# Kernel optimization log

Hardware: AMD Instinct MI355X
Metric: run time of the kernel (lower is better)

The kernel has to match this reference:

```python
import jax, jax.numpy as jnp
import numpy as np

NEG_FILL = -1000000.0


def setup_inputs() -> dict:
    key = jax.random.key(0)
    k1, k2, k3, k4, k5 = jax.random.split(key, 5)
    bs, sl, hd, dd = 128, 512, 1024, 512
    x = jax.random.normal(k1, (bs, sl, hd), dtype=jnp.float32)
    mask = jax.random.randint(k2, (bs, sl), 0, 2) > 0  # bool, True = masked out
    Wq = jax.random.normal(k3, (dd, hd), dtype=jnp.float32)
    bq = jax.random.normal(k4, (dd,), dtype=jnp.float32)
    vq = jax.random.normal(k5, (dd,), dtype=jnp.float32)
    return {"x": x, "mask": mask, "Wq": Wq, "bq": bq, "vq": vq}


def reference(x, mask, Wq, bq, vq):
    # key = tanh(Uq(x)): [bs, sl, dd]
    k = jnp.tanh(jnp.einsum("bsh,dh->bsd", x, Wq) + bq)
    # score = vq . key: [bs, sl]
    score = jnp.einsum("bsd,d->bs", k, vq)
    score = jnp.where(mask, NEG_FILL, score)
    weight = jax.nn.softmax(score, axis=-1)  # [bs, sl]
    # weighted sum over sequence: [bs, hd]
    res = jnp.einsum("bs,bsh->bh", weight, x)
    return res
```

## Files before the change

kernel.cpp:

```cpp
#include <hip/hip_runtime.h>
#include <stdint.h>

#define BS 128
#define SL 512
#define HD 1024
#define DD 512
#define M_TOT (BS*SL)

typedef __attribute__((ext_vector_type(8))) short short8;
typedef __attribute__((ext_vector_type(4))) float f32x4;

__device__ __forceinline__ unsigned short f32_bf16(float f) {
    union { float f; unsigned u; } v; v.f = f;
    unsigned u = v.u + 0x7FFFu + ((v.u >> 16) & 1u);
    return (unsigned short)(u >> 16);
}
__device__ __forceinline__ float bf16_f32(unsigned short h) {
    union { unsigned u; float f; } v; v.u = ((unsigned)h) << 16; return v.f;
}
__device__ __forceinline__ float fast_tanh(float x) {
    float e = __expf(2.0f * x);
    return 1.0f - 2.0f / (e + 1.0f);
}
__device__ __forceinline__ void async_lds16(const void* g, void* l) {
    __builtin_amdgcn_global_load_lds(
        (const __attribute__((address_space(1))) unsigned int*)g,
        (__attribute__((address_space(3))) unsigned int*)l, 16, 0, 0);
}

__global__ void pack_wq_kernel(const float* __restrict__ Wq,
                               unsigned short* __restrict__ P,
                               const unsigned* __restrict__ mw,
                               int* __restrict__ flag) {
    if (blockIdx.x == 0) {
        unsigned bad = 0;
        for (int i = threadIdx.x; i < 1024; i += 256) bad |= (mw[i] > 1u) ? 1u : 0u;
        if (bad) atomicExch(flag, 1);
    }
    int t = blockIdx.x * 256 + threadIdx.x;
    int d  = t >> 7;
    int h0 = (t & 127) << 3;
    const float* src = Wq + (size_t)d * HD + h0;
    union { unsigned short s[8]; uint4 v; } a, b;
#pragma unroll
    for (int j = 0; j < 8; ++j) {
        float f = src[j];
        a.s[j] = f32_bf16(f);
        b.s[j] = f32_bf16(f - bf16_f32(a.s[j]));
    }
    int nb = d >> 7, cg = (d >> 4) & 7, lr = d & 15;
    int ks = h0 >> 5, q = (h0 >> 3) & 3;
    int l = q * 16 + lr;
    size_t base = (size_t)(nb * 32 + ks) * 8192 + (size_t)(cg * 64 + l) * 8;
    *(uint4*)(P + base)        = a.v;
    *(uint4*)(P + base + 4096) = b.v;
}

__launch_bounds__(256, 3)
__global__ void score_kernel(const float* __restrict__ x,
                             const unsigned short* __restrict__ packW,
                             const float* __restrict__ bq,
                             const float* __restrict__ vq,
                             float* __restrict__ score) {
    __shared__ unsigned short A_hi[4096];
    __shared__ unsigned short A_lo[4096];
    __shared__ unsigned short Bt[8192];

    const int bid = blockIdx.x;
    const int xcd = bid & 7;
    const int slot = bid >> 3;
    const int nb = slot & 3;
    const int m0 = (xcd + ((slot >> 2) << 3)) << 7;

    const int t = threadIdx.x;
    const int l = t & 63;
    const int w = t >> 6;
    const int wm = w & 1, wn = w >> 1;

    f32x4 acc[4][4];
#pragma unroll
    for (int i = 0; i < 4; ++i)
#pragma unroll
        for (int j = 0; j < 4; ++j)
            acc[i][j] = (f32x4){0.f, 0.f, 0.f, 0.f};

    const char* Ahc = (const char*)A_hi;
    const char* Alc = (const char*)A_lo;

    int arow[2], ac8[2];
#pragma unroll
    for (int r = 0; r < 2; ++r) {
        int u = r * 256 + t;
        arow[r] = u >> 2; ac8[r] = u & 3;
    }

    float4 px[2][2];
#pragma unroll
    for (int r = 0; r < 2; ++r) {
        const float4* xp = (const float4*)(x + (size_t)(m0 + arow[r]) * HD + ac8[r] * 8);
        px[r][0] = xp[0]; px[r][1] = xp[1];
    }

    for (int ks = 0; ks < 32; ++ks) {
        __syncthreads();
        {
            const unsigned short* src = packW + (size_t)(nb * 32 + ks) * 8192;
#pragma unroll
            for (int r = 0; r < 4; ++r)
                async_lds16(src + (size_t)(r * 256 + t) * 8, Bt + (r * 256 + t) * 8);
        }
#pragma unroll
        for (int r = 0; r < 2; ++r) {
            float4 v0 = px[r][0], v1 = px[r][1];
            float ff[8] = {v0.x, v0.y, v0.z, v0.w, v1.x, v1.y, v1.z, v1.w};
            union { unsigned short s[8]; uint4 q4; } hi, lo;
#pragma unroll
            for (int j = 0; j < 8; ++j) {
                hi.s[j] = f32_bf16(ff[j]);
                lo.s[j] = f32_bf16(ff[j] - bf16_f32(hi.s[j]));
            }
            int rg = arow[r] >> 4, rr = arow[r] & 15;
            int off = (((rg * 64 + ac8[r] * 16 + rr) * 16) ^ (ac8[r] << 5));
            *(uint4*)((char*)A_hi + off) = hi.q4;
            *(uint4*)((char*)A_lo + off) = lo.q4;
        }
        __syncthreads();

        if (ks < 31) {
#pragma unroll
            for (int r = 0; r < 2; ++r) {
                const float4* xp = (const float4*)(x + (size_t)(m0 + arow[r]) * HD
                                                   + (ks + 1) * 32 + ac8[r] * 8);
                px[r][0] = xp[0]; px[r][1] = xp[1];
            }
        }

        const short8* Bh = (const short8*)Bt;
        const short8* Bl = (const short8*)(Bt + 4096);
        short8 ah[4], al[4], bh[4], bl[4];
        const int xr = (l >> 4) << 5;
#pragma unroll
        for (int i = 0; i < 4; ++i) {
            int off = ((((wm * 4 + i) * 64 + l) * 16) ^ xr);
            ah[i] = *(const short8*)(Ahc + off);
            al[i] = *(const short8*)(Alc + off);
        }
#pragma unroll
        for (int j = 0; j < 4; ++j) {
            bh[j] = Bh[(wn * 4 + j) * 64 + l];
            bl[j] = Bl[(wn * 4 + j) * 64 + l];
        }
#pragma unroll
        for (int i = 0; i < 4; ++i)
#pragma unroll
            for (int j = 0; j < 4; ++j) {
                acc[i][j] = __builtin_amdgcn_mfma_f32_16x16x32_bf16(ah[i], bh[j], acc[i][j], 0, 0, 0);
                acc[i][j] = __builtin_amdgcn_mfma_f32_16x16x32_bf16(al[i], bh[j], acc[i][j], 0, 0, 0);
                acc[i][j] = __builtin_amdgcn_mfma_f32_16x16x32_bf16(ah[i], bl[j], acc[i][j], 0, 0, 0);
            }
    }

    int q = l >> 4, c = l & 15;
#pragma unroll
    for (int i = 0; i < 4; ++i) {
        float rs[4] = {0.f, 0.f, 0.f, 0.f};
#pragma unroll
        for (int j = 0; j < 4; ++j) {
            int n = nb * 128 + wn * 64 + j * 16 + c;
            float bqv = bq[n], vqv = vq[n];
            f32x4 a4 = acc[i][j];
#pragma unroll
            for (int r = 0; r < 4; ++r)
                rs[r] += fast_tanh(a4[r] + bqv) * vqv;
        }
#pragma unroll
        for (int r = 0; r < 4; ++r) {
            float v = rs[r];
            v += __shfl_xor(v, 1);
            v += __shfl_xor(v, 2);
            v += __shfl_xor(v, 4);
            v += __shfl_xor(v, 8);
            if (c == 0)
                atomicAdd(&score[m0 + wm * 64 + i * 16 + q * 4 + r], v);
        }
    }
}

__global__ void softmax_kernel(const float* __restrict__ score,
                               const void* __restrict__ maskp,
                               const int* __restrict__ flag,
                               float* __restrict__ wgt) {
    __shared__ float red[8];
    int b = blockIdx.x, t = threadIdx.x;
    int w = t >> 6, l = t & 63;
    bool u8 = (*flag != 0);
    int i0 = b * SL + t, i1 = i0 + 256;
    bool mk0, mk1;
    if (u8) {
        mk0 = ((const unsigned char*)maskp)[i0] != 0;
        mk1 = ((const unsigned char*)maskp)[i1] != 0;
    } else {
        mk0 = ((const int*)maskp)[i0] != 0;
        mk1 = ((const int*)maskp)[i1] != 0;
    }
    float s0 = mk0 ? -1000000.0f : score[i0];
    float s1 = mk1 ? -1000000.0f : score[i1];
    float mx = fmaxf(s0, s1);
    for (int d = 1; d < 64; d <<= 1) mx = fmaxf(mx, __shfl_xor(mx, d));
    if (l == 0) red[w] = mx;
    __syncthreads();
    mx = fmaxf(fmaxf(red[0], red[1]), fmaxf(red[2], red[3]));
    float e0 = expf(s0 - mx), e1 = expf(s1 - mx);
    float sm = e0 + e1;
    for (int d = 1; d < 64; d <<= 1) sm += __shfl_xor(sm, d);
    if (l == 0) red[4 + w] = sm;
    __syncthreads();
    sm = red[4] + red[5] + red[6] + red[7];
    float inv = 1.0f / sm;
    wgt[i0] = e0 * inv;
    wgt[i1] = e1 * inv;
}

__global__ void wsum_partial_kernel(const float* __restrict__ x,
                                    const float* __restrict__ wgt,
                                    float* __restrict__ partial) {
    __shared__ float wsh[64];
    int b = blockIdx.x, sc = blockIdx.y, t = threadIdx.x;
    if (t < 64) wsh[t] = wgt[b * SL + sc * 64 + t];
    __syncthreads();
    const float4* xp = (const float4*)(x + ((size_t)b * SL + sc * 64) * HD) + t;
    float ax = 0.f, ay = 0.f, az = 0.f, aw = 0.f;
#pragma unroll 4
    for (int s = 0; s < 64; ++s) {
        float wv = wsh[s];
        float4 v = xp[(size_t)s * 256];
        ax += wv * v.x; ay += wv * v.y; az += wv * v.z; aw += wv * v.w;
    }
    float4 r = {ax, ay, az, aw};
    ((float4*)(partial + (size_t)(b * 8 + sc) * HD))[t] = r;
}

__global__ void wsum_reduce_kernel(const float* __restrict__ partial,
                                   float* __restrict__ out) {
    int i = blockIdx.x * 256 + threadIdx.x;
    int b = i >> 8, h4 = i & 255;
    const float4* p = (const float4*)partial + (size_t)b * 8 * 256 + h4;
    float4 a = p[0];
#pragma unroll
    for (int sc = 1; sc < 8; ++sc) {
        float4 v = p[sc * 256];
        a.x += v.x; a.y += v.y; a.z += v.z; a.w += v.w;
    }
    ((float4*)out)[i] = a;
}

extern "C" void kernel_launch(void* const* d_in, const int* in_sizes, int n_in,
                              void* d_out, int out_size, void* d_ws, size_t ws_size,
                              hipStream_t stream) {
    const float* x  = (const float*)d_in[0];
    const void* mask = d_in[1];
    const float* Wq = (const float*)d_in[2];
    const float* bq = (const float*)d_in[3];
    const float* vq = (const float*)d_in[4];
    float* out = (float*)d_out;

    char* ws = (char*)d_ws;
    unsigned short* packW = (unsigned short*)ws;
    float* score   = (float*)(ws + (2u << 20));
    int*   flag    = (int*)  (ws + (2u << 20) + (256u << 10));
    float* wgt     = (float*)(ws + (2u << 20) + (257u << 10));
    float* partial = (float*)(ws + (3u << 20));

    hipMemsetAsync(score, 0, (256u << 10) + 4, stream);

    pack_wq_kernel<<<256, 256, 0, stream>>>(Wq, packW, (const unsigned*)mask, flag);
    score_kernel<<<2048, 256, 0, stream>>>(x, packW, bq, vq, score);
    softmax_kernel<<<BS, 256, 0, stream>>>(score, mask, flag, wgt);
    wsum_partial_kernel<<<dim3(BS, 8), 256, 0, stream>>>(x, wgt, partial);
    wsum_reduce_kernel<<<128, 256, 0, stream>>>(partial, out);
}
```

Measured before the change: 523.5 us.

## Fuse softmax and weighted sum into one kernel and use packed bf16 conversion

Merges the softmax, partial weighted-sum and reduce kernels into a single attend kernel. Each of the 8 blocks per batch recomputes the full softmax redundantly and accumulates its partial result into a zeroed output with atomics, which removes two launches and the wgt/partial round trips through memory. The score kernel's bf16 hi/lo split now uses the packed v_cvt_pk_bf16_f32 instruction, and the swizzled LDS offset is hoisted out of the k loop. The costs are extra memset and atomic traffic on the output, plus nondeterministic summation order.

```diff
diff --git a/kernel.cpp b/kernel.cpp
--- a/kernel.cpp
+++ b/kernel.cpp
@@ -17,6 +17,11 @@
 }
 __device__ __forceinline__ float bf16_f32(unsigned short h) {
     union { unsigned u; float f; } v; v.u = ((unsigned)h) << 16; return v.f;
+}
+__device__ __forceinline__ unsigned cvt_pk_bf16(float a, float b) {
+    unsigned r;
+    asm("v_cvt_pk_bf16_f32 %0, %1, %2" : "=v"(r) : "v"(a), "v"(b));
+    return r;
 }
 __device__ __forceinline__ float fast_tanh(float x) {
     float e = __expf(2.0f * x);
@@ -87,11 +92,13 @@
     const char* Ahc = (const char*)A_hi;
     const char* Alc = (const char*)A_lo;
 
-    int arow[2], ac8[2];
+    int arow[2], ac8[2], aoff[2];
 #pragma unroll
     for (int r = 0; r < 2; ++r) {
         int u = r * 256 + t;
         arow[r] = u >> 2; ac8[r] = u & 3;
+        int rg = arow[r] >> 4, rr = arow[r] & 15;
+        aoff[r] = (((rg * 64 + ac8[r] * 16 + rr) * 16) ^ (ac8[r] << 5));
     }
 
     float4 px[2][2];
@@ -113,16 +120,21 @@
         for (int r = 0; r < 2; ++r) {
             float4 v0 = px[r][0], v1 = px[r][1];
             float ff[8] = {v0.x, v0.y, v0.z, v0.w, v1.x, v1.y, v1.z, v1.w};
-            union { unsigned short s[8]; uint4 q4; } hi, lo;
-#pragma unroll
-            for (int j = 0; j < 8; ++j) {
-                hi.s[j] = f32_bf16(ff[j]);
-                lo.s[j] = f32_bf16(ff[j] - bf16_f32(hi.s[j]));
+            unsigned hw[4], lw[4];
+#pragma unroll
+            for (int jj = 0; jj < 4; ++jj) {
+                float f0 = ff[2 * jj], f1 = ff[2 * jj + 1];
+                unsigned h = cvt_pk_bf16(f0, f1);
+                hw[jj] = h;
+                union { unsigned u; float f; } c0, c1;
+                c0.u = h << 16;
+                c1.u = h & 0xFFFF0000u;
+                lw[jj] = cvt_pk_bf16(f0 - c0.f, f1 - c1.f);
             }
-            int rg = arow[r] >> 4, rr = arow[r] & 15;
-            int off = (((rg * 64 + ac8[r] * 16 + rr) * 16) ^ (ac8[r] << 5));
-            *(uint4*)((char*)A_hi + off) = hi.q4;
-            *(uint4*)((char*)A_lo + off) = lo.q4;
+            uint4 hv = {hw[0], hw[1], hw[2], hw[3]};
+            uint4 lv = {lw[0], lw[1], lw[2], lw[3]};
+            *(uint4*)((char*)A_hi + aoff[r]) = hv;
+            *(uint4*)((char*)A_lo + aoff[r]) = lv;
         }
         __syncthreads();
 
@@ -186,13 +198,15 @@
     }
 }
 
-__global__ void softmax_kernel(const float* __restrict__ score,
-                               const void* __restrict__ maskp,
-                               const int* __restrict__ flag,
-                               float* __restrict__ wgt) {
+__global__ void attend_kernel(const float* __restrict__ x,
+                              const float* __restrict__ score,
+                              const void* __restrict__ maskp,
+                              const int* __restrict__ flag,
+                              float* __restrict__ out) {
     __shared__ float red[8];
-    int b = blockIdx.x, t = threadIdx.x;
-    int w = t >> 6, l = t & 63;
+    __shared__ float wsh[SL];
+    int b = blockIdx.x, sc = blockIdx.y, t = threadIdx.x;
+    int w = t >> 6;
     bool u8 = (*flag != 0);
     int i0 = b * SL + t, i1 = i0 + 256;
     bool mk0, mk1;
@@ -207,51 +221,34 @@
     float s1 = mk1 ? -1000000.0f : score[i1];
     float mx = fmaxf(s0, s1);
     for (int d = 1; d < 64; d <<= 1) mx = fmaxf(mx, __shfl_xor(mx, d));
-    if (l == 0) red[w] = mx;
+    if ((t & 63) == 0) red[w] = mx;
     __syncthreads();
     mx = fmaxf(fmaxf(red[0], red[1]), fmaxf(red[2], red[3]));
     float e0 = expf(s0 - mx), e1 = expf(s1 - mx);
     float sm = e0 + e1;
     for (int d = 1; d < 64; d <<= 1) sm += __shfl_xor(sm, d);
-    if (l == 0) red[4 + w] = sm;
+    if ((t & 63) == 0) red[4 + w] = sm;
     __syncthreads();
     sm = red[4] + red[5] + red[6] + red[7];
     float inv = 1.0f / sm;
-    wgt[i0] = e0 * inv;
-    wgt[i1] = e1 * inv;
-}
-
-__global__ void wsum_partial_kernel(const float* __restrict__ x,
-                                    const float* __restrict__ wgt,
-                                    float* __restrict__ partial) {
-    __shared__ float wsh[64];
-    int b = blockIdx.x, sc = blockIdx.y, t = threadIdx.x;
-    if (t < 64) wsh[t] = wgt[b * SL + sc * 64 + t];
+    wsh[t] = e0 * inv;
+    wsh[t + 256] = e1 * inv;
     __syncthreads();
+
+    const float* wp = wsh + sc * 64;
     const float4* xp = (const float4*)(x + ((size_t)b * SL + sc * 64) * HD) + t;
     float ax = 0.f, ay = 0.f, az = 0.f, aw = 0.f;
 #pragma unroll 4
     for (int s = 0; s < 64; ++s) {
-        float wv = wsh[s];
+        float wv = wp[s];
         float4 v = xp[(size_t)s * 256];
         ax += wv * v.x; ay += wv * v.y; az += wv * v.z; aw += wv * v.w;
     }
-    float4 r = {ax, ay, az, aw};
-    ((float4*)(partial + (size_t)(b * 8 + sc) * HD))[t] = r;
-}
-
-__global__ void wsum_reduce_kernel(const float* __restrict__ partial,
-                                   float* __restrict__ out) {
-    int i = blockIdx.x * 256 + threadIdx.x;
-    int b = i >> 8, h4 = i & 255;
-    const float4* p = (const float4*)partial + (size_t)b * 8 * 256 + h4;
-    float4 a = p[0];
-#pragma unroll
-    for (int sc = 1; sc < 8; ++sc) {
-        float4 v = p[sc * 256];
-        a.x += v.x; a.y += v.y; a.z += v.z; a.w += v.w;
-    }
-    ((float4*)out)[i] = a;
+    float* op = out + (size_t)b * HD + t * 4;
+    atomicAdd(op + 0, ax);
+    atomicAdd(op + 1, ay);
+    atomicAdd(op + 2, az);
+    atomicAdd(op + 3, aw);
 }
 
 extern "C" void kernel_launch(void* const* d_in, const int* in_sizes, int n_in,
@@ -268,14 +265,11 @@
     unsigned short* packW = (unsigned short*)ws;
     float* score   = (float*)(ws + (2u << 20));
     int*   flag    = (int*)  (ws + (2u << 20) + (256u << 10));
-    float* wgt     = (float*)(ws + (2u << 20) + (257u << 10));
-    float* partial = (float*)(ws + (3u << 20));
 
     hipMemsetAsync(score, 0, (256u << 10) + 4, stream);
+    hipMemsetAsync(out, 0, (size_t)BS * HD * sizeof(float), stream);
 
     pack_wq_kernel<<<256, 256, 0, stream>>>(Wq, packW, (const unsigned*)mask, flag);
     score_kernel<<<2048, 256, 0, stream>>>(x, packW, bq, vq, score);
-    softmax_kernel<<<BS, 256, 0, stream>>>(score, mask, flag, wgt);
-    wsum_partial_kernel<<<dim3(BS, 8), 256, 0, stream>>>(x, wgt, partial);
-    wsum_reduce_kernel<<<128, 256, 0, stream>>>(partial, out);
-}
+    attend_kernel<<<dim3(BS, 8), 256, 0, stream>>>(x, score, mask, flag, out);
+}
```

Result: slower. 567.6 us (+8.4%).
